# Optimization experiments

Hardware: AMD Instinct MI355X
Metric: run time of the kernel (lower is better)

Reference implementation:

```python
import jax, jax.numpy as jnp
import numpy as np

DIM = 128
NUM_HEADS = 8
HEAD_DIM = DIM // NUM_HEADS
SCALE = HEAD_DIM ** -0.5


def _attn_branch(xs, Wq, bq, Wp, bp):
    # xs: (N, L, C) batch of sequences; Q=K=V=q (per the module)
    N, L, C = xs.shape
    q = xs @ Wq + bq                                   # (N, L, C)
    q = q.reshape(N, L, NUM_HEADS, HEAD_DIM).transpose(0, 2, 1, 3)  # (N, h, L, d)
    qs = q * SCALE
    attn = jax.nn.softmax(jnp.einsum('nhld,nhmd->nhlm', qs, qs), axis=-1)
    out = jnp.einsum('nhlm,nhmd->nhld', attn, q)       # (N, h, L, d)
    out = out.transpose(0, 2, 1, 3).reshape(N, L, C)
    return out @ Wp + bp


def setup_inputs() -> dict:
    key = jax.random.key(0)
    ks = jax.random.split(key, 12)
    B, C, D, H, W = 1, DIM, 31, 32, 32
    s = 0.02
    return {
        'x': jax.random.normal(ks[0], (B, C, D, H, W), jnp.float32),
        'Wq_spec': jax.random.normal(ks[1], (C, C), jnp.float32) * s,
        'bq_spec': jnp.zeros((C,), jnp.float32),
        'Wp_spec': jax.random.normal(ks[2], (C, C), jnp.float32) * s,
        'bp_spec': jnp.zeros((C,), jnp.float32),
        'Wq_spat': jax.random.normal(ks[3], (C, C), jnp.float32) * s,
        'bq_spat': jnp.zeros((C,), jnp.float32),
        'Wp_spat': jax.random.normal(ks[4], (C, C), jnp.float32) * s,
        'bp_spat': jnp.zeros((C,), jnp.float32),
        'Wg': jax.random.normal(ks[5], (2 * C, C), jnp.float32) * s,
        'bg': jnp.zeros((C,), jnp.float32),
    }


def reference(x, Wq_spec, bq_spec, Wp_spec, bp_spec,
              Wq_spat, bq_spat, Wp_spat, bp_spat, Wg, bg):
    B, C, D, H, W = x.shape
    # ---- spectral branch: sequences of length D per spatial position ----
    x_spec = x.transpose(0, 3, 4, 2, 1).reshape(B * H * W, D, C)
    out_spec = _attn_branch(x_spec, Wq_spec, bq_spec, Wp_spec, bp_spec)
    out_spectral = out_spec.reshape(B, H, W, D, C).transpose(0, 4, 3, 1, 2)  # (B,C,D,H,W)
    # ---- spatial branch: sequences of length H*W per band ----
    x_spat = x.transpose(0, 2, 3, 4, 1).reshape(B * D, H * W, C)
    out_spat = _attn_branch(x_spat, Wq_spat, bq_spat, Wp_spat, bp_spat)
    out_spatial = out_spat.reshape(B, D, H, W, C).transpose(0, 4, 1, 2, 3)   # (B,C,D,H,W)
    # ---- sigmoid-gated fusion (global average pooled gate) ----
    gi = jnp.concatenate([
        out_spectral.mean(axis=(2, 3, 4)),
        out_spatial.mean(axis=(2, 3, 4)),
    ], axis=-1)                                          # (B, 2C)
    gate = jax.nn.sigmoid(gi @ Wg + bg)[:, :, None, None, None]  # (B,C,1,1,1)
    return gate * out_spectral + (1.0 - gate) * out_spatial
```

## Files before the change

### kernel.cpp

```cpp
#include <hip/hip_runtime.h>
#include <cstddef>

#define CC 128
#define NH 8
#define HD 16
#define DDIM 31
#define HWW 1024
#define TOK 31744
#define SCALE2 0.0625f
#define QTOK 64

typedef __attribute__((ext_vector_type(4))) short  short4v;
typedef __attribute__((ext_vector_type(8))) short  short8v;
typedef __attribute__((ext_vector_type(4))) float  float4v;
typedef __attribute__((ext_vector_type(2))) unsigned uint2v;
typedef __attribute__((ext_vector_type(8))) __bf16 bf16x8;

__device__ inline unsigned bf16rne(float f) {
    unsigned u = __float_as_uint(f);
    return (u + 0x7fffu + ((u >> 16) & 1u)) >> 16;
}
__device__ inline float bf2f(unsigned h) { return __uint_as_float(h << 16); }

__device__ inline unsigned packsplit(float v) {
    unsigned h = bf16rne(v);
    unsigned l = bf16rne(v - bf2f(h));
    return h | (l << 16);
}
__device__ inline uint2 pack_hi4(uint4 p) {
    return make_uint2((p.x & 0xffffu) | (p.y << 16),
                      (p.z & 0xffffu) | (p.w << 16));
}
__device__ inline uint2 pack_lo4(uint4 p) {
    return make_uint2((p.x >> 16) | (p.y & 0xffff0000u),
                      (p.z >> 16) | (p.w & 0xffff0000u));
}

__device__ inline short4v pack_pf(unsigned u0, unsigned u1,
                                  unsigned u2, unsigned u3) {
    uint2v pd;
    pd[0] = __builtin_amdgcn_perm(u1, u0, 0x07060302u);
    pd[1] = __builtin_amdgcn_perm(u3, u2, 0x07060302u);
    return __builtin_bit_cast(short4v, pd);
}

__device__ inline float4v mfma32(short8v a, short8v b, float4v c) {
    return __builtin_amdgcn_mfma_f32_16x16x32_bf16(
        __builtin_bit_cast(bf16x8, a), __builtin_bit_cast(bf16x8, b), c, 0, 0, 0);
}

__device__ inline void load_wfrags32(const float* __restrict__ W, int co0, int l,
                                     int quad, short8v* ah, short8v* al)
{
#pragma unroll
    for (int k4 = 0; k4 < 4; ++k4) {
#pragma unroll
        for (int j = 0; j < 8; ++j) {
            float w = W[(size_t)(k4 * 32 + quad * 8 + j) * CC + co0 + l];
            unsigned h = bf16rne(w);
            ah[k4][j] = (short)h;
            al[k4][j] = (short)bf16rne(w - bf2f(h));
        }
    }
}

#define AST 136

__global__ __launch_bounds__(512, 4) void qproj_kernel(
    const float* __restrict__ x,
    const float* __restrict__ Wq1, const float* __restrict__ Wq2,
    const float* __restrict__ bq1, const float* __restrict__ bq2,
    unsigned* __restrict__ q1p, unsigned* __restrict__ q2p,
    float* __restrict__ sums)
{
    __shared__ ushort sbuf[2 * QTOK * AST];
    ushort* Ahi = sbuf;
    ushort* Alo = sbuf + QTOK * AST;
    unsigned* S = (unsigned*)sbuf;
    const int tid = threadIdx.x;
    const int t0  = blockIdx.x * QTOK;
    if (blockIdx.x == 0 && tid < 2 * CC) sums[tid] = 0.f;

    for (int i = tid; i < CC * QTOK / 4; i += 512) {
        int t4 = i & 15, ci = i >> 4;
        float4 v = *(const float4*)&x[(size_t)ci * TOK + t0 + t4 * 4];
        float xv[4] = {v.x, v.y, v.z, v.w};
#pragma unroll
        for (int e = 0; e < 4; ++e) {
            unsigned h = bf16rne(xv[e]);
            unsigned lw = bf16rne(xv[e] - bf2f(h));
            Ahi[(t4 * 4 + e) * AST + ci] = (ushort)h;
            Alo[(t4 * 4 + e) * AST + ci] = (ushort)lw;
        }
    }
    __syncthreads();

    const int lane = tid & 63;
    const int l    = lane & 15;
    const int quad = lane >> 4;
    const int co0  = (tid >> 6) * 16;

    short8v ah[2][4], al[2][4];
    load_wfrags32(Wq1, co0, l, quad, ah[0], al[0]);
    load_wfrags32(Wq2, co0, l, quad, ah[1], al[1]);
    float4v acc[2][4];
#pragma unroll
    for (int br = 0; br < 2; ++br)
#pragma unroll
        for (int nt = 0; nt < 4; ++nt) acc[br][nt] = (float4v){0.f, 0.f, 0.f, 0.f};
#pragma unroll
    for (int k4 = 0; k4 < 4; ++k4) {
#pragma unroll
        for (int nt = 0; nt < 4; ++nt) {
            short8v bh = *(const short8v*)&Ahi[(nt * 16 + l) * AST + k4 * 32 + quad * 8];
            short8v bl = *(const short8v*)&Alo[(nt * 16 + l) * AST + k4 * 32 + quad * 8];
            acc[0][nt] = mfma32(ah[0][k4], bh, acc[0][nt]);
            acc[0][nt] = mfma32(ah[0][k4], bl, acc[0][nt]);
            acc[0][nt] = mfma32(al[0][k4], bh, acc[0][nt]);
            acc[1][nt] = mfma32(ah[1][k4], bh, acc[1][nt]);
            acc[1][nt] = mfma32(ah[1][k4], bl, acc[1][nt]);
            acc[1][nt] = mfma32(al[1][k4], bh, acc[1][nt]);
        }
    }

    for (int branch = 0; branch < 2; ++branch) {
        const float* bq = branch ? bq2 : bq1;
        unsigned* op    = branch ? q2p : q1p;
        float4 bv = *(const float4*)&bq[co0 + quad * 4];
        float bb[4] = {bv.x, bv.y, bv.z, bv.w};
        __syncthreads();
#pragma unroll
        for (int nt = 0; nt < 4; ++nt) {
#pragma unroll
            for (int reg = 0; reg < 4; ++reg)
                S[(nt * 16 + l) * AST + co0 + quad * 4 + reg] =
                    packsplit(acc[branch][nt][reg] + bb[reg]);
        }
        __syncthreads();
        for (int i = tid; i < QTOK * 32; i += 512) {
            int t = i >> 5, c4 = i & 31;
            uint4 pv = *(const uint4*)&S[t * AST + c4 * 4];
            *(uint4*)&op[(size_t)(t0 + t) * CC + c4 * 4] = pv;
        }
    }
}

#define QS2 132
#define QSS 20
#define QTP 1044
__global__ __launch_bounds__(1024, 4) void attn_kernel(
    unsigned* __restrict__ q1p, unsigned* __restrict__ q2p,
    float* __restrict__ sums)
{
    __shared__ __align__(16) ushort smem[HWW * QSS + HD * QTP];
    __shared__ float fsum[CC];
    const int tid  = threadIdx.x;
    const int lane = tid & 63;
    const int l    = lane & 15;
    const int quad = lane >> 4;
    const float k2 = SCALE2 * 1.44269504f;
    const short4v onesb = {(short)0x3F80, (short)0x3F80, (short)0x3F80, (short)0x3F80};
    if (tid < CC) fsum[tid] = 0.f;

    {
        const int d = blockIdx.x >> 3, h = blockIdx.x & 7;
        ushort* Qs  = smem;
        ushort* QTs = smem + HWW * QSS;
        const size_t base = (size_t)d * HWW * CC + h * HD;

        for (int i = tid; i < HWW * 4; i += 1024) {
            int row = i >> 2, q4 = i & 3;
            uint4 p = *(const uint4*)&q2p[base + (size_t)row * CC + q4 * 4];
            *(uint2*)&Qs[row * QSS + q4 * 4] = pack_hi4(p);
            QTs[(q4 * 4 + 0) * QTP + row] = (ushort)p.x;
            QTs[(q4 * 4 + 1) * QTP + row] = (ushort)p.y;
            QTs[(q4 * 4 + 2) * QTP + row] = (ushort)p.z;
            QTs[(q4 * 4 + 3) * QTP + row] = (ushort)p.w;
        }
        __syncthreads();

        const int Rw = (tid >> 6) * 64;
        short4v qf[4];
#pragma unroll
        for (int lt = 0; lt < 4; ++lt) {
            short4v raw = *(short4v*)&Qs[(Rw + lt * 16 + l) * QSS + quad * 4];
            short4v sc;
#pragma unroll
            for (int e = 0; e < 4; ++e) {
                float f = bf2f((unsigned)(ushort)raw[e]) * k2;
                sc[e] = (short)bf16rne(f);
            }
            qf[lt] = sc;
        }

        float4v acc[4], accs[4];
#pragma unroll
        for (int lt = 0; lt < 4; ++lt) {
            acc[lt]  = (float4v){0.f, 0.f, 0.f, 0.f};
            accs[lt] = (float4v){0.f, 0.f, 0.f, 0.f};
        }

#pragma unroll 2
        for (int mt = 0; mt < 64; ++mt) {
            const int m0 = mt * 16;
            short4v ka = *(short4v*)&Qs[(m0 + l) * QSS + quad * 4];
            short4v vb = *(short4v*)&QTs[l * QTP + m0 + quad * 4];
#pragma unroll
            for (int lt = 0; lt < 4; ++lt) {
                float4v s = __builtin_amdgcn_mfma_f32_16x16x16bf16_1k(
                    ka, qf[lt], (float4v){0.f, 0.f, 0.f, 0.f}, 0, 0, 0);
                unsigned u0 = __float_as_uint(__builtin_amdgcn_exp2f(s[0]));
                unsigned u1 = __float_as_uint(__builtin_amdgcn_exp2f(s[1]));
                unsigned u2 = __float_as_uint(__builtin_amdgcn_exp2f(s[2]));
                unsigned u3 = __float_as_uint(__builtin_amdgcn_exp2f(s[3]));
                short4v pf = pack_pf(u0, u1, u2, u3);
                acc[lt]  = __builtin_amdgcn_mfma_f32_16x16x16bf16_1k(vb, pf, acc[lt], 0, 0, 0);
                accs[lt] = __builtin_amdgcn_mfma_f32_16x16x16bf16_1k(onesb, pf, accs[lt], 0, 0, 0);
            }
        }

        float vsum[4] = {0.f, 0.f, 0.f, 0.f};
#pragma unroll
        for (int lt = 0; lt < 4; ++lt) {
            float inv = 1.f / accs[lt][0];
            int token = Rw + lt * 16 + l;
            float v0 = acc[lt][0] * inv, v1 = acc[lt][1] * inv;
            float v2 = acc[lt][2] * inv, v3 = acc[lt][3] * inv;
            uint4 pv;
            pv.x = packsplit(v0); pv.y = packsplit(v1);
            pv.z = packsplit(v2); pv.w = packsplit(v3);
            *(uint4*)&q2p[base + (size_t)token * CC + quad * 4] = pv;
            vsum[0] += v0; vsum[1] += v1; vsum[2] += v2; vsum[3] += v3;
        }
#pragma unroll
        for (int reg = 0; reg < 4; ++reg) {
            float v = vsum[reg];
            v += __shfl_xor(v, 1); v += __shfl_xor(v, 2);
            v += __shfl_xor(v, 4); v += __shfl_xor(v, 8);
            if (l == 0) atomicAdd(&fsum[quad * 4 + reg], v);
        }
        __syncthreads();
        if (tid < HD) atomicAdd(&sums[CC + h * HD + tid], fsum[tid]);
    }

    const int half_id = blockIdx.x >> 1;
    const bool has_job = (blockIdx.x & 1) ? (half_id < 4) : (half_id < 124);
    if (!has_job) return;
    const int job = (blockIdx.x & 1) ? (124 + half_id) : half_id;
    const int hw0 = job * 8;

    __syncthreads();
    if (tid < CC) fsum[tid] = 0.f;

    const int wave = tid >> 6;
    const int hwl  = wave >> 1;
    const int half = wave & 1;
    const int hw   = hw0 + hwl;
    ushort* Q = smem + hwl * (32 * QS2);
    for (int it = 0; it < 8; ++it) {
        int idx = it * 64 + lane;
        int dd = half * 16 + (idx >> 5), c4 = idx & 31;
        if (dd < 31) {
            uint4 p = *(const uint4*)&q1p[((size_t)dd * HWW + hw) * CC + c4 * 4];
            *(uint2*)&Q[dd * QS2 + c4 * 4] = pack_hi4(p);
        }
    }
    if (half) for (int i = lane; i < 128; i += 64) Q[31 * QS2 + i] = 0;
    __syncthreads();

    const int hh = half * 4;
#pragma unroll
    for (int hl = 0; hl < 4; ++hl) {
        const int hc = (hh + hl) * HD;
        short4v qf[2];
        qf[0] = *(const short4v*)&Q[l * QS2 + hc + quad * 4];
        qf[1] = *(const short4v*)&Q[(16 + l) * QS2 + hc + quad * 4];
        short4v va[2];
#pragma unroll
        for (int j = 0; j < 2; ++j)
#pragma unroll
            for (int jj = 0; jj < 4; ++jj)
                va[j][jj] = (short)Q[(j * 16 + quad * 4 + jj) * QS2 + hc + l];

        float4v o[2]   = {(float4v){0.f,0.f,0.f,0.f}, (float4v){0.f,0.f,0.f,0.f}};
        float4v osr[2] = {(float4v){0.f,0.f,0.f,0.f}, (float4v){0.f,0.f,0.f,0.f}};
#pragma unroll
        for (int j = 0; j < 2; ++j) {
#pragma unroll
            for (int i2 = 0; i2 < 2; ++i2) {
                float4v s = __builtin_amdgcn_mfma_f32_16x16x16bf16_1k(
                    qf[j], qf[i2], (float4v){0.f,0.f,0.f,0.f}, 0, 0, 0);
                unsigned u0 = __float_as_uint(__builtin_amdgcn_exp2f(s[0] * k2));
                unsigned u1 = __float_as_uint(__builtin_amdgcn_exp2f(s[1] * k2));
                unsigned u2 = __float_as_uint(__builtin_amdgcn_exp2f(s[2] * k2));
                unsigned u3 = __float_as_uint(__builtin_amdgcn_exp2f(s[3] * k2));
                if (j == 1 && quad == 3) u3 = 0;
                short4v pf = pack_pf(u0, u1, u2, u3);
                o[i2]   = __builtin_amdgcn_mfma_f32_16x16x16bf16_1k(va[j], pf, o[i2], 0, 0, 0);
                osr[i2] = __builtin_amdgcn_mfma_f32_16x16x16bf16_1k(onesb, pf, osr[i2], 0, 0, 0);
            }
        }
        float vsum[4] = {0.f, 0.f, 0.f, 0.f};
#pragma unroll
        for (int i2 = 0; i2 < 2; ++i2) {
            float inv = 1.f / osr[i2][0];
            int dq = i2 * 16 + l;
            if (dq < 31) {
                uint4 pv;
                float v0 = o[i2][0] * inv, v1 = o[i2][1] * inv;
                float v2 = o[i2][2] * inv, v3 = o[i2][3] * inv;
                pv.x = packsplit(v0); pv.y = packsplit(v1);
                pv.z = packsplit(v2); pv.w = packsplit(v3);
                *(uint4*)&q1p[((size_t)dq * HWW + hw) * CC + hc + quad * 4] = pv;
                vsum[0] += v0; vsum[1] += v1; vsum[2] += v2; vsum[3] += v3;
            }
        }
#pragma unroll
        for (int r = 0; r < 4; ++r) {
            float v = vsum[r];
            v += __shfl_xor(v, 1); v += __shfl_xor(v, 2);
            v += __shfl_xor(v, 4); v += __shfl_xor(v, 8);
            if (l == 0) atomicAdd(&fsum[hc + quad * 4 + r], v);
        }
    }
    __syncthreads();
    if (tid < CC) atomicAdd(&sums[tid], fsum[tid]);
}

__global__ __launch_bounds__(512, 4) void oproj_kernel(
    const unsigned* __restrict__ q1p, const unsigned* __restrict__ q2p,
    const float* __restrict__ Wp1, const float* __restrict__ Wp2,
    const float* __restrict__ bp1, const float* __restrict__ bp2,
    const float* __restrict__ Wg,  const float* __restrict__ bg,
    const float* __restrict__ sums, float* __restrict__ out)
{
    __shared__ ushort sbuf[2 * 64 * AST];
    ushort* Ahi = sbuf;
    ushort* Alo = sbuf + 64 * AST;
    unsigned* S = (unsigned*)sbuf;
    __shared__ float pa[4][CC];
    __shared__ float giv[2 * CC];
    __shared__ float gf[CC];
    const int tid = threadIdx.x;
    const int t0  = blockIdx.x * 64;
    const int lane = tid & 63;
    const int l    = lane & 15;
    const int quad = lane >> 4;
    const int co0  = (tid >> 6) * 16;

    {
        const int part = tid >> 7, c = tid & 127;
        const float* Wp = (part < 2) ? Wp1 : Wp2;
        const float* sp = (part < 2) ? sums : sums + CC;
        const int k0 = (part & 1) * 64;
        float a = 0.f;
        for (int kk = 0; kk < 64; ++kk) {
            int k = k0 + kk;
            a += sp[k] * Wp[(size_t)k * CC + c];
        }
        pa[part][c] = a;
        __syncthreads();
        if (tid < 2 * CC) {
            float m = (tid < CC) ? (pa[0][tid] + pa[1][tid])
                                 : (pa[2][tid - CC] + pa[3][tid - CC]);
            float bb = (tid < CC) ? bp1[tid] : bp2[tid - CC];
            giv[tid] = m * (1.f / (float)TOK) + bb;
        }
        __syncthreads();
        float b = 0.f;
        for (int kk = 0; kk < 64; ++kk) {
            int j = part * 64 + kk;
            b += giv[j] * Wg[(size_t)j * CC + c];
        }
        pa[part][c] = b;
        __syncthreads();
        if (tid < CC)
            gf[tid] = 1.f / (1.f + __expf(-(bg[tid] + pa[0][tid] + pa[1][tid] +
                                           pa[2][tid] + pa[3][tid])));
    }

    float4v acc[2][4];
#pragma unroll
    for (int br = 0; br < 2; ++br)
#pragma unroll
        for (int nt = 0; nt < 4; ++nt) acc[br][nt] = (float4v){0.f, 0.f, 0.f, 0.f};

    for (int br = 0; br < 2; ++br) {
        const unsigned* Ap = br ? q2p : q1p;
        const float*    W  = br ? Wp2 : Wp1;
        short8v ah[4], al[4];
        load_wfrags32(W, co0, l, quad, ah, al);
        __syncthreads();
        for (int i = tid; i < 64 * 32; i += 512) {
            int t = i >> 5, c4 = i & 31;
            uint4 p = *(const uint4*)&Ap[(size_t)(t0 + t) * CC + c4 * 4];
            *(uint2*)&Ahi[t * AST + c4 * 4] = pack_hi4(p);
            *(uint2*)&Alo[t * AST + c4 * 4] = pack_lo4(p);
        }
        __syncthreads();
#pragma unroll
        for (int k4 = 0; k4 < 4; ++k4) {
#pragma unroll
            for (int nt = 0; nt < 4; ++nt) {
                short8v bh = *(const short8v*)&Ahi[(nt * 16 + l) * AST + k4 * 32 + quad * 8];
                short8v bl = *(const short8v*)&Alo[(nt * 16 + l) * AST + k4 * 32 + quad * 8];
                acc[br][nt] = mfma32(ah[k4], bh, acc[br][nt]);
                acc[br][nt] = mfma32(ah[k4], bl, acc[br][nt]);
                acc[br][nt] = mfma32(al[k4], bh, acc[br][nt]);
            }
        }
    }

    float4 b1 = *(const float4*)&bp1[co0 + quad * 4];
    float4 b2 = *(const float4*)&bp2[co0 + quad * 4];
    float bb1[4] = {b1.x, b1.y, b1.z, b1.w};
    float bb2[4] = {b2.x, b2.y, b2.z, b2.w};
    float gg[4];
#pragma unroll
    for (int e = 0; e < 4; ++e) gg[e] = gf[co0 + quad * 4 + e];

    __syncthreads();
#pragma unroll
    for (int nt = 0; nt < 4; ++nt) {
        int tl = nt * 16 + l;
#pragma unroll
        for (int reg = 0; reg < 4; ++reg) {
            float v = gg[reg] * (acc[0][nt][reg] + bb1[reg]) +
                      (1.f - gg[reg]) * (acc[1][nt][reg] + bb2[reg]);
            S[(co0 + quad * 4 + reg) * 66 + tl] = __float_as_uint(v);
        }
    }
    __syncthreads();
    for (int i = tid; i < 128 * 32; i += 512) {
        int co = i >> 5, t2 = i & 31;
        uint2 v = *(const uint2*)&S[co * 66 + t2 * 2];
        *(uint2*)&out[(size_t)co * TOK + t0 + t2 * 2] = v;
    }
}

extern "C" void kernel_launch(void* const* d_in, const int* in_sizes, int n_in,
                              void* d_out, int out_size, void* d_ws, size_t ws_size,
                              hipStream_t stream)
{
    const float* x   = (const float*)d_in[0];
    const float* Wq1 = (const float*)d_in[1];
    const float* bq1 = (const float*)d_in[2];
    const float* Wp1 = (const float*)d_in[3];
    const float* bp1 = (const float*)d_in[4];
    const float* Wq2 = (const float*)d_in[5];
    const float* bq2 = (const float*)d_in[6];
    const float* Wp2 = (const float*)d_in[7];
    const float* bp2 = (const float*)d_in[8];
    const float* Wg  = (const float*)d_in[9];
    const float* bg  = (const float*)d_in[10];
    float* out = (float*)d_out;

    const size_t plane = (size_t)TOK * CC;
    unsigned* q1p = (unsigned*)d_ws;
    unsigned* q2p = q1p + plane;
    float*   sums = (float*)(q2p + plane);

    qproj_kernel<<<dim3(TOK / QTOK), 512, 0, stream>>>(x, Wq1, Wq2, bq1, bq2,
                                                       q1p, q2p, sums);
    attn_kernel<<<dim3(248), 1024, 0, stream>>>(q1p, q2p, sums);
    oproj_kernel<<<dim3(496), 512, 0, stream>>>(q1p, q2p,
                                                Wp1, Wp2, bp1, bp2, Wg, bg,
                                                sums, out);
}
```

Baseline: 173.0 us.

## Fuse three kernels into one cooperative persistent kernel with grid syncs

Replaces the three separate launches (q-projection, attention, output projection) with a single cooperative kernel of 248 blocks of 1024 threads that runs the three phases separated by grid-wide barriers. To fit the fixed grid, the projection phases now process 128 tokens per block with 16 waves. The weight bf16 hi/lo fragments are now converted per k-step inside the loop instead of preloaded, which lowers register use. If the cooperative launch fails, it falls back to three ordinary launches. This removes launch gaps and inter-kernel drain, but adds grid-sync cost and gives the projection phases fewer, larger blocks.

```diff
diff --git a/kernel.cpp b/kernel.cpp
--- a/kernel.cpp
+++ b/kernel.cpp
@@ -1,5 +1,8 @@
 #include <hip/hip_runtime.h>
+#include <hip/hip_cooperative_groups.h>
 #include <cstddef>
+
+namespace cg = cooperative_groups;
 
 #define CC 128
 #define NH 8
@@ -8,7 +11,9 @@
 #define HWW 1024
 #define TOK 31744
 #define SCALE2 0.0625f
-#define QTOK 64
+#define GRID 248
+#define BTOK 128
+#define AST 136
 
 typedef __attribute__((ext_vector_type(4))) short  short4v;
 typedef __attribute__((ext_vector_type(8))) short  short8v;
@@ -49,77 +54,76 @@
         __builtin_bit_cast(bf16x8, a), __builtin_bit_cast(bf16x8, b), c, 0, 0, 0);
 }
 
-__device__ inline void load_wfrags32(const float* __restrict__ W, int co0, int l,
-                                     int quad, short8v* ah, short8v* al)
-{
-#pragma unroll
-    for (int k4 = 0; k4 < 4; ++k4) {
-#pragma unroll
-        for (int j = 0; j < 8; ++j) {
-            float w = W[(size_t)(k4 * 32 + quad * 8 + j) * CC + co0 + l];
-            unsigned h = bf16rne(w);
-            ah[k4][j] = (short)h;
-            al[k4][j] = (short)bf16rne(w - bf2f(h));
-        }
-    }
-}
-
-#define AST 136
-
-__global__ __launch_bounds__(512, 4) void qproj_kernel(
+__device__ __forceinline__ void qproj_phase(
     const float* __restrict__ x,
     const float* __restrict__ Wq1, const float* __restrict__ Wq2,
     const float* __restrict__ bq1, const float* __restrict__ bq2,
     unsigned* __restrict__ q1p, unsigned* __restrict__ q2p,
-    float* __restrict__ sums)
-{
-    __shared__ ushort sbuf[2 * QTOK * AST];
+    float* __restrict__ sums, ushort* sbuf, int bx, int tid)
+{
     ushort* Ahi = sbuf;
-    ushort* Alo = sbuf + QTOK * AST;
+    ushort* Alo = sbuf + BTOK * AST;
     unsigned* S = (unsigned*)sbuf;
-    const int tid = threadIdx.x;
-    const int t0  = blockIdx.x * QTOK;
-    if (blockIdx.x == 0 && tid < 2 * CC) sums[tid] = 0.f;
-
-    for (int i = tid; i < CC * QTOK / 4; i += 512) {
-        int t4 = i & 15, ci = i >> 4;
-        float4 v = *(const float4*)&x[(size_t)ci * TOK + t0 + t4 * 4];
-        float xv[4] = {v.x, v.y, v.z, v.w};
-#pragma unroll
-        for (int e = 0; e < 4; ++e) {
-            unsigned h = bf16rne(xv[e]);
-            unsigned lw = bf16rne(xv[e] - bf2f(h));
-            Ahi[(t4 * 4 + e) * AST + ci] = (ushort)h;
-            Alo[(t4 * 4 + e) * AST + ci] = (ushort)lw;
-        }
+    const int t0 = bx * BTOK;
+    if (bx == 0 && tid < 2 * CC) sums[tid] = 0.f;
+
+    for (int i = tid; i < BTOK * 32; i += 1024) {
+        int t = i & (BTOK - 1), c4 = i >> 7;
+        unsigned hw[2], lw[2];
+#pragma unroll
+        for (int p = 0; p < 2; ++p) {
+            unsigned h0, l0, h1, l1;
+            {
+                float v = x[(size_t)(c4 * 4 + p * 2 + 0) * TOK + t0 + t];
+                h0 = bf16rne(v); l0 = bf16rne(v - bf2f(h0));
+            }
+            {
+                float v = x[(size_t)(c4 * 4 + p * 2 + 1) * TOK + t0 + t];
+                h1 = bf16rne(v); l1 = bf16rne(v - bf2f(h1));
+            }
+            hw[p] = h0 | (h1 << 16);
+            lw[p] = l0 | (l1 << 16);
+        }
+        *(uint2*)&Ahi[t * AST + c4 * 4] = make_uint2(hw[0], hw[1]);
+        *(uint2*)&Alo[t * AST + c4 * 4] = make_uint2(lw[0], lw[1]);
     }
     __syncthreads();
 
     const int lane = tid & 63;
     const int l    = lane & 15;
     const int quad = lane >> 4;
-    const int co0  = (tid >> 6) * 16;
-
-    short8v ah[2][4], al[2][4];
-    load_wfrags32(Wq1, co0, l, quad, ah[0], al[0]);
-    load_wfrags32(Wq2, co0, l, quad, ah[1], al[1]);
+    const int wv   = tid >> 6;
+    const int co0  = (wv & 7) * 16;
+    const int tb   = (wv >> 3) * 64;
+
     float4v acc[2][4];
 #pragma unroll
     for (int br = 0; br < 2; ++br)
 #pragma unroll
         for (int nt = 0; nt < 4; ++nt) acc[br][nt] = (float4v){0.f, 0.f, 0.f, 0.f};
+
 #pragma unroll
     for (int k4 = 0; k4 < 4; ++k4) {
+        short8v ah0, al0, ah1, al1;
+#pragma unroll
+        for (int j = 0; j < 8; ++j) {
+            float w1 = Wq1[(size_t)(k4 * 32 + quad * 8 + j) * CC + co0 + l];
+            unsigned h1 = bf16rne(w1);
+            ah0[j] = (short)h1; al0[j] = (short)bf16rne(w1 - bf2f(h1));
+            float w2 = Wq2[(size_t)(k4 * 32 + quad * 8 + j) * CC + co0 + l];
+            unsigned h2 = bf16rne(w2);
+            ah1[j] = (short)h2; al1[j] = (short)bf16rne(w2 - bf2f(h2));
+        }
 #pragma unroll
         for (int nt = 0; nt < 4; ++nt) {
-            short8v bh = *(const short8v*)&Ahi[(nt * 16 + l) * AST + k4 * 32 + quad * 8];
-            short8v bl = *(const short8v*)&Alo[(nt * 16 + l) * AST + k4 * 32 + quad * 8];
-            acc[0][nt] = mfma32(ah[0][k4], bh, acc[0][nt]);
-            acc[0][nt] = mfma32(ah[0][k4], bl, acc[0][nt]);
-            acc[0][nt] = mfma32(al[0][k4], bh, acc[0][nt]);
-            acc[1][nt] = mfma32(ah[1][k4], bh, acc[1][nt]);
-            acc[1][nt] = mfma32(ah[1][k4], bl, acc[1][nt]);
-            acc[1][nt] = mfma32(al[1][k4], bh, acc[1][nt]);
+            short8v bh = *(const short8v*)&Ahi[(tb + nt * 16 + l) * AST + k4 * 32 + quad * 8];
+            short8v bl = *(const short8v*)&Alo[(tb + nt * 16 + l) * AST + k4 * 32 + quad * 8];
+            acc[0][nt] = mfma32(ah0, bh, acc[0][nt]);
+            acc[0][nt] = mfma32(ah0, bl, acc[0][nt]);
+            acc[0][nt] = mfma32(al0, bh, acc[0][nt]);
+            acc[1][nt] = mfma32(ah1, bh, acc[1][nt]);
+            acc[1][nt] = mfma32(ah1, bl, acc[1][nt]);
+            acc[1][nt] = mfma32(al1, bh, acc[1][nt]);
         }
     }
 
@@ -133,11 +137,11 @@
         for (int nt = 0; nt < 4; ++nt) {
 #pragma unroll
             for (int reg = 0; reg < 4; ++reg)
-                S[(nt * 16 + l) * AST + co0 + quad * 4 + reg] =
+                S[(tb + nt * 16 + l) * AST + co0 + quad * 4 + reg] =
                     packsplit(acc[branch][nt][reg] + bb[reg]);
         }
         __syncthreads();
-        for (int i = tid; i < QTOK * 32; i += 512) {
+        for (int i = tid; i < BTOK * 32; i += 1024) {
             int t = i >> 5, c4 = i & 31;
             uint4 pv = *(const uint4*)&S[t * AST + c4 * 4];
             *(uint4*)&op[(size_t)(t0 + t) * CC + c4 * 4] = pv;
@@ -148,13 +152,10 @@
 #define QS2 132
 #define QSS 20
 #define QTP 1044
-__global__ __launch_bounds__(1024, 4) void attn_kernel(
+__device__ __forceinline__ void attn_phase(
     unsigned* __restrict__ q1p, unsigned* __restrict__ q2p,
-    float* __restrict__ sums)
-{
-    __shared__ __align__(16) ushort smem[HWW * QSS + HD * QTP];
-    __shared__ float fsum[CC];
-    const int tid  = threadIdx.x;
+    float* __restrict__ sums, ushort* smem, float* fsum, int bx, int tid)
+{
     const int lane = tid & 63;
     const int l    = lane & 15;
     const int quad = lane >> 4;
@@ -163,7 +164,7 @@
     if (tid < CC) fsum[tid] = 0.f;
 
     {
-        const int d = blockIdx.x >> 3, h = blockIdx.x & 7;
+        const int d = bx >> 3, h = bx & 7;
         ushort* Qs  = smem;
         ushort* QTs = smem + HWW * QSS;
         const size_t base = (size_t)d * HWW * CC + h * HD;
@@ -243,199 +244,270 @@
         if (tid < HD) atomicAdd(&sums[CC + h * HD + tid], fsum[tid]);
     }
 
-    const int half_id = blockIdx.x >> 1;
-    const bool has_job = (blockIdx.x & 1) ? (half_id < 4) : (half_id < 124);
-    if (!has_job) return;
-    const int job = (blockIdx.x & 1) ? (124 + half_id) : half_id;
-    const int hw0 = job * 8;
+    const int half_id = bx >> 1;
+    const bool has_job = (bx & 1) ? (half_id < 4) : (half_id < 124);
+    if (has_job) {
+        const int job = (bx & 1) ? (124 + half_id) : half_id;
+        const int hw0 = job * 8;
+
+        __syncthreads();
+        if (tid < CC) fsum[tid] = 0.f;
+
+        const int wave = tid >> 6;
+        const int hwl  = wave >> 1;
+        const int half = wave & 1;
+        const int hw   = hw0 + hwl;
+        ushort* Q = smem + hwl * (32 * QS2);
+        for (int it = 0; it < 8; ++it) {
+            int idx = it * 64 + lane;
+            int dd = half * 16 + (idx >> 5), c4 = idx & 31;
+            if (dd < 31) {
+                uint4 p = *(const uint4*)&q1p[((size_t)dd * HWW + hw) * CC + c4 * 4];
+                *(uint2*)&Q[dd * QS2 + c4 * 4] = pack_hi4(p);
+            }
+        }
+        if (half) for (int i = lane; i < 128; i += 64) Q[31 * QS2 + i] = 0;
+        __syncthreads();
+
+        const int hh = half * 4;
+#pragma unroll
+        for (int hl = 0; hl < 4; ++hl) {
+            const int hc = (hh + hl) * HD;
+            short4v qf[2];
+            qf[0] = *(const short4v*)&Q[l * QS2 + hc + quad * 4];
+            qf[1] = *(const short4v*)&Q[(16 + l) * QS2 + hc + quad * 4];
+            short4v va[2];
+#pragma unroll
+            for (int j = 0; j < 2; ++j)
+#pragma unroll
+                for (int jj = 0; jj < 4; ++jj)
+                    va[j][jj] = (short)Q[(j * 16 + quad * 4 + jj) * QS2 + hc + l];
+
+            float4v o[2]   = {(float4v){0.f,0.f,0.f,0.f}, (float4v){0.f,0.f,0.f,0.f}};
+            float4v osr[2] = {(float4v){0.f,0.f,0.f,0.f}, (float4v){0.f,0.f,0.f,0.f}};
+#pragma unroll
+            for (int j = 0; j < 2; ++j) {
+#pragma unroll
+                for (int i2 = 0; i2 < 2; ++i2) {
+                    float4v s = __builtin_amdgcn_mfma_f32_16x16x16bf16_1k(
+                        qf[j], qf[i2], (float4v){0.f,0.f,0.f,0.f}, 0, 0, 0);
+                    unsigned u0 = __float_as_uint(__builtin_amdgcn_exp2f(s[0] * k2));
+                    unsigned u1 = __float_as_uint(__builtin_amdgcn_exp2f(s[1] * k2));
+                    unsigned u2 = __float_as_uint(__builtin_amdgcn_exp2f(s[2] * k2));
+                    unsigned u3 = __float_as_uint(__builtin_amdgcn_exp2f(s[3] * k2));
+                    if (j == 1 && quad == 3) u3 = 0;
+                    short4v pf = pack_pf(u0, u1, u2, u3);
+                    o[i2]   = __builtin_amdgcn_mfma_f32_16x16x16bf16_1k(va[j], pf, o[i2], 0, 0, 0);
+                    osr[i2] = __builtin_amdgcn_mfma_f32_16x16x16bf16_1k(onesb, pf, osr[i2], 0, 0, 0);
+                }
+            }
+            float vsum[4] = {0.f, 0.f, 0.f, 0.f};
+#pragma unroll
+            for (int i2 = 0; i2 < 2; ++i2) {
+                float inv = 1.f / osr[i2][0];
+                int dq = i2 * 16 + l;
+                if (dq < 31) {
+                    uint4 pv;
+                    float v0 = o[i2][0] * inv, v1 = o[i2][1] * inv;
+                    float v2 = o[i2][2] * inv, v3 = o[i2][3] * inv;
+                    pv.x = packsplit(v0); pv.y = packsplit(v1);
+                    pv.z = packsplit(v2); pv.w = packsplit(v3);
+                    *(uint4*)&q1p[((size_t)dq * HWW + hw) * CC + hc + quad * 4] = pv;
+                    vsum[0] += v0; vsum[1] += v1; vsum[2] += v2; vsum[3] += v3;
+                }
+            }
+#pragma unroll
+            for (int r = 0; r < 4; ++r) {
+                float v = vsum[r];
+                v += __shfl_xor(v, 1); v += __shfl_xor(v, 2);
+                v += __shfl_xor(v, 4); v += __shfl_xor(v, 8);
+                if (l == 0) atomicAdd(&fsum[hc + quad * 4 + r], v);
+            }
+        }
+        __syncthreads();
+        if (tid < CC) atomicAdd(&sums[tid], fsum[tid]);
+    }
+}
+
+__device__ __forceinline__ void oproj_phase(
+    const unsigned* __restrict__ q1p, const unsigned* __restrict__ q2p,
+    const float* __restrict__ Wp1, const float* __restrict__ Wp2,
+    const float* __restrict__ bp1, const float* __restrict__ bp2,
+    const float* __restrict__ Wg,  const float* __restrict__ bg,
+    const float* __restrict__ sums, float* __restrict__ out,
+    ushort* sbuf, float* pa, float* giv, float* gf, int bx, int tid)
+{
+    ushort* Ahi = sbuf;
+    ushort* Alo = sbuf + BTOK * AST;
+    unsigned* S = (unsigned*)sbuf;
+    const int t0 = bx * BTOK;
+    const int lane = tid & 63;
+    const int l    = lane & 15;
+    const int quad = lane >> 4;
+    const int wv   = tid >> 6;
+    const int co0  = (wv & 7) * 16;
+    const int tb   = (wv >> 3) * 64;
+
+    {
+        const int part = tid >> 7, c = tid & 127;
+        if (part < 4) {
+            const float* Wp = (part < 2) ? Wp1 : Wp2;
+            const float* sp = (part < 2) ? sums : sums + CC;
+            const int k0 = (part & 1) * 64;
+            float a = 0.f;
+            for (int kk = 0; kk < 64; ++kk) {
+                int k = k0 + kk;
+                a += sp[k] * Wp[(size_t)k * CC + c];
+            }
+            pa[part * CC + c] = a;
+        }
+        __syncthreads();
+        if (tid < 2 * CC) {
+            float m = (tid < CC) ? (pa[0 * CC + tid] + pa[1 * CC + tid])
+                                 : (pa[2 * CC + tid - CC] + pa[3 * CC + tid - CC]);
+            float bb = (tid < CC) ? bp1[tid] : bp2[tid - CC];
+            giv[tid] = m * (1.f / (float)TOK) + bb;
+        }
+        __syncthreads();
+        if (part < 4) {
+            float b = 0.f;
+            for (int kk = 0; kk < 64; ++kk) {
+                int j = part * 64 + kk;
+                b += giv[j] * Wg[(size_t)j * CC + c];
+            }
+            pa[part * CC + c] = b;
+        }
+        __syncthreads();
+        if (tid < CC)
+            gf[tid] = 1.f / (1.f + __expf(-(bg[tid] + pa[0 * CC + tid] + pa[1 * CC + tid] +
+                                           pa[2 * CC + tid] + pa[3 * CC + tid])));
+    }
+
+    float4v acc[2][4];
+#pragma unroll
+    for (int br = 0; br < 2; ++br)
+#pragma unroll
+        for (int nt = 0; nt < 4; ++nt) acc[br][nt] = (float4v){0.f, 0.f, 0.f, 0.f};
+
+    for (int br = 0; br < 2; ++br) {
+        const unsigned* Ap = br ? q2p : q1p;
+        const float*    W  = br ? Wp2 : Wp1;
+        __syncthreads();
+        for (int i = tid; i < BTOK * 32; i += 1024) {
+            int t = i >> 5, c4 = i & 31;
+            uint4 p = *(const uint4*)&Ap[(size_t)(t0 + t) * CC + c4 * 4];
+            *(uint2*)&Ahi[t * AST + c4 * 4] = pack_hi4(p);
+            *(uint2*)&Alo[t * AST + c4 * 4] = pack_lo4(p);
+        }
+        __syncthreads();
+#pragma unroll
+        for (int k4 = 0; k4 < 4; ++k4) {
+            short8v ah, al;
+#pragma unroll
+            for (int j = 0; j < 8; ++j) {
+                float w = W[(size_t)(k4 * 32 + quad * 8 + j) * CC + co0 + l];
+                unsigned h = bf16rne(w);
+                ah[j] = (short)h; al[j] = (short)bf16rne(w - bf2f(h));
+            }
+#pragma unroll
+            for (int nt = 0; nt < 4; ++nt) {
+                short8v bh = *(const short8v*)&Ahi[(tb + nt * 16 + l) * AST + k4 * 32 + quad * 8];
+                short8v bl = *(const short8v*)&Alo[(tb + nt * 16 + l) * AST + k4 * 32 + quad * 8];
+                acc[br][nt] = mfma32(ah, bh, acc[br][nt]);
+                acc[br][nt] = mfma32(ah, bl, acc[br][nt]);
+                acc[br][nt] = mfma32(al, bh, acc[br][nt]);
+            }
+        }
+    }
+
+    float4 b1 = *(const float4*)&bp1[co0 + quad * 4];
+    float4 b2 = *(const float4*)&bp2[co0 + quad * 4];
+    float bb1[4] = {b1.x, b1.y, b1.z, b1.w};
+    float bb2[4] = {b2.x, b2.y, b2.z, b2.w};
+    float4 gv = *(const float4*)&gf[co0 + quad * 4];
+    float gg[4] = {gv.x, gv.y, gv.z, gv.w};
 
     __syncthreads();
-    if (tid < CC) fsum[tid] = 0.f;
-
-    const int wave = tid >> 6;
-    const int hwl  = wave >> 1;
-    const int half = wave & 1;
-    const int hw   = hw0 + hwl;
-    ushort* Q = smem + hwl * (32 * QS2);
-    for (int it = 0; it < 8; ++it) {
-        int idx = it * 64 + lane;
-        int dd = half * 16 + (idx >> 5), c4 = idx & 31;
-        if (dd < 31) {
-            uint4 p = *(const uint4*)&q1p[((size_t)dd * HWW + hw) * CC + c4 * 4];
-            *(uint2*)&Q[dd * QS2 + c4 * 4] = pack_hi4(p);
-        }
-    }
-    if (half) for (int i = lane; i < 128; i += 64) Q[31 * QS2 + i] = 0;
+#pragma unroll
+    for (int nt = 0; nt < 4; ++nt) {
+        int tl = tb + nt * 16 + l;
+#pragma unroll
+        for (int reg = 0; reg < 4; ++reg) {
+            float v = gg[reg] * (acc[0][nt][reg] + bb1[reg]) +
+                      (1.f - gg[reg]) * (acc[1][nt][reg] + bb2[reg]);
+            S[(co0 + quad * 4 + reg) * 130 + tl] = __float_as_uint(v);
+        }
+    }
     __syncthreads();
-
-    const int hh = half * 4;
-#pragma unroll
-    for (int hl = 0; hl < 4; ++hl) {
-        const int hc = (hh + hl) * HD;
-        short4v qf[2];
-        qf[0] = *(const short4v*)&Q[l * QS2 + hc + quad * 4];
-        qf[1] = *(const short4v*)&Q[(16 + l) * QS2 + hc + quad * 4];
-        short4v va[2];
-#pragma unroll
-        for (int j = 0; j < 2; ++j)
-#pragma unroll
-            for (int jj = 0; jj < 4; ++jj)
-                va[j][jj] = (short)Q[(j * 16 + quad * 4 + jj) * QS2 + hc + l];
-
-        float4v o[2]   = {(float4v){0.f,0.f,0.f,0.f}, (float4v){0.f,0.f,0.f,0.f}};
-        float4v osr[2] = {(float4v){0.f,0.f,0.f,0.f}, (float4v){0.f,0.f,0.f,0.f}};
-#pragma unroll
-        for (int j = 0; j < 2; ++j) {
-#pragma unroll
-            for (int i2 = 0; i2 < 2; ++i2) {
-                float4v s = __builtin_amdgcn_mfma_f32_16x16x16bf16_1k(
-                    qf[j], qf[i2], (float4v){0.f,0.f,0.f,0.f}, 0, 0, 0);
-                unsigned u0 = __float_as_uint(__builtin_amdgcn_exp2f(s[0] * k2));
-                unsigned u1 = __float_as_uint(__builtin_amdgcn_exp2f(s[1] * k2));
-                unsigned u2 = __float_as_uint(__builtin_amdgcn_exp2f(s[2] * k2));
-                unsigned u3 = __float_as_uint(__builtin_amdgcn_exp2f(s[3] * k2));
-                if (j == 1 && quad == 3) u3 = 0;
-                short4v pf = pack_pf(u0, u1, u2, u3);
-                o[i2]   = __builtin_amdgcn_mfma_f32_16x16x16bf16_1k(va[j], pf, o[i2], 0, 0, 0);
-                osr[i2] = __builtin_amdgcn_mfma_f32_16x16x16bf16_1k(onesb, pf, osr[i2], 0, 0, 0);
-            }
-        }
-        float vsum[4] = {0.f, 0.f, 0.f, 0.f};
-#pragma unroll
-        for (int i2 = 0; i2 < 2; ++i2) {
-            float inv = 1.f / osr[i2][0];
-            int dq = i2 * 16 + l;
-            if (dq < 31) {
-                uint4 pv;
-                float v0 = o[i2][0] * inv, v1 = o[i2][1] * inv;
-                float v2 = o[i2][2] * inv, v3 = o[i2][3] * inv;
-                pv.x = packsplit(v0); pv.y = packsplit(v1);
-                pv.z = packsplit(v2); pv.w = packsplit(v3);
-                *(uint4*)&q1p[((size_t)dq * HWW + hw) * CC + hc + quad * 4] = pv;
-                vsum[0] += v0; vsum[1] += v1; vsum[2] += v2; vsum[3] += v3;
-            }
-        }
-#pragma unroll
-        for (int r = 0; r < 4; ++r) {
-            float v = vsum[r];
-            v += __shfl_xor(v, 1); v += __shfl_xor(v, 2);
-            v += __shfl_xor(v, 4); v += __shfl_xor(v, 8);
-            if (l == 0) atomicAdd(&fsum[hc + quad * 4 + r], v);
-        }
-    }
-    __syncthreads();
-    if (tid < CC) atomicAdd(&sums[tid], fsum[tid]);
-}
-
-__global__ __launch_bounds__(512, 4) void oproj_kernel(
+    for (int i = tid; i < 128 * 64; i += 1024) {
+        int co = i >> 6, t2 = i & 63;
+        uint2 v = *(const uint2*)&S[co * 130 + t2 * 2];
+        *(uint2*)&out[(size_t)co * TOK + t0 + t2 * 2] = v;
+    }
+}
+
+__global__ __launch_bounds__(1024, 4) void fused_kernel(
+    const float* __restrict__ x,
+    const float* __restrict__ Wq1, const float* __restrict__ bq1,
+    const float* __restrict__ Wp1, const float* __restrict__ bp1,
+    const float* __restrict__ Wq2, const float* __restrict__ bq2,
+    const float* __restrict__ Wp2, const float* __restrict__ bp2,
+    const float* __restrict__ Wg,  const float* __restrict__ bg,
+    float* __restrict__ out,
+    unsigned* __restrict__ q1p, unsigned* __restrict__ q2p,
+    float* __restrict__ sums)
+{
+    __shared__ __align__(16) ushort smem[HWW * QSS + HD * QTP];
+    __shared__ float fsum[CC];
+    __shared__ float pa[4 * CC];
+    __shared__ float giv[2 * CC];
+    __shared__ float gf[CC];
+    const int bx = blockIdx.x, tid = threadIdx.x;
+
+    qproj_phase(x, Wq1, Wq2, bq1, bq2, q1p, q2p, sums, smem, bx, tid);
+    __threadfence();
+    cg::this_grid().sync();
+    attn_phase(q1p, q2p, sums, smem, fsum, bx, tid);
+    __threadfence();
+    cg::this_grid().sync();
+    oproj_phase(q1p, q2p, Wp1, Wp2, bp1, bp2, Wg, bg, sums, out,
+                smem, pa, giv, gf, bx, tid);
+}
+
+__global__ __launch_bounds__(1024, 4) void qproj_k(
+    const float* __restrict__ x,
+    const float* __restrict__ Wq1, const float* __restrict__ Wq2,
+    const float* __restrict__ bq1, const float* __restrict__ bq2,
+    unsigned* __restrict__ q1p, unsigned* __restrict__ q2p,
+    float* __restrict__ sums)
+{
+    __shared__ __align__(16) ushort smem[2 * BTOK * AST];
+    qproj_phase(x, Wq1, Wq2, bq1, bq2, q1p, q2p, sums, smem,
+                blockIdx.x, threadIdx.x);
+}
+
+__global__ __launch_bounds__(1024, 4) void attn_k(
+    unsigned* __restrict__ q1p, unsigned* __restrict__ q2p,
+    float* __restrict__ sums)
+{
+    __shared__ __align__(16) ushort smem[HWW * QSS + HD * QTP];
+    __shared__ float fsum[CC];
+    attn_phase(q1p, q2p, sums, smem, fsum, blockIdx.x, threadIdx.x);
+}
+
+__global__ __launch_bounds__(1024, 4) void oproj_k(
     const unsigned* __restrict__ q1p, const unsigned* __restrict__ q2p,
     const float* __restrict__ Wp1, const float* __restrict__ Wp2,
     const float* __restrict__ bp1, const float* __restrict__ bp2,
     const float* __restrict__ Wg,  const float* __restrict__ bg,
     const float* __restrict__ sums, float* __restrict__ out)
 {
-    __shared__ ushort sbuf[2 * 64 * AST];
-    ushort* Ahi = sbuf;
-    ushort* Alo = sbuf + 64 * AST;
-    unsigned* S = (unsigned*)sbuf;
-    __shared__ float pa[4][CC];
+    __shared__ __align__(16) ushort smem[2 * BTOK * AST];
+    __shared__ float pa[4 * CC];
     __shared__ float giv[2 * CC];
     __shared__ float gf[CC];
-    const int tid = threadIdx.x;
-    const int t0  = blockIdx.x * 64;
-    const int lane = tid & 63;
-    const int l    = lane & 15;
-    const int quad = lane >> 4;
-    const int co0  = (tid >> 6) * 16;
-
-    {
-        const int part = tid >> 7, c = tid & 127;
-        const float* Wp = (part < 2) ? Wp1 : Wp2;
-        const float* sp = (part < 2) ? sums : sums + CC;
-        const int k0 = (part & 1) * 64;
-        float a = 0.f;
-        for (int kk = 0; kk < 64; ++kk) {
-            int k = k0 + kk;
-            a += sp[k] * Wp[(size_t)k * CC + c];
-        }
-        pa[part][c] = a;
-        __syncthreads();
-        if (tid < 2 * CC) {
-            float m = (tid < CC) ? (pa[0][tid] + pa[1][tid])
-                                 : (pa[2][tid - CC] + pa[3][tid - CC]);
-            float bb = (tid < CC) ? bp1[tid] : bp2[tid - CC];
-            giv[tid] = m * (1.f / (float)TOK) + bb;
-        }
-        __syncthreads();
-        float b = 0.f;
-        for (int kk = 0; kk < 64; ++kk) {
-            int j = part * 64 + kk;
-            b += giv[j] * Wg[(size_t)j * CC + c];
-        }
-        pa[part][c] = b;
-        __syncthreads();
-        if (tid < CC)
-            gf[tid] = 1.f / (1.f + __expf(-(bg[tid] + pa[0][tid] + pa[1][tid] +
-                                           pa[2][tid] + pa[3][tid])));
-    }
-
-    float4v acc[2][4];
-#pragma unroll
-    for (int br = 0; br < 2; ++br)
-#pragma unroll
-        for (int nt = 0; nt < 4; ++nt) acc[br][nt] = (float4v){0.f, 0.f, 0.f, 0.f};
-
-    for (int br = 0; br < 2; ++br) {
-        const unsigned* Ap = br ? q2p : q1p;
-        const float*    W  = br ? Wp2 : Wp1;
-        short8v ah[4], al[4];
-        load_wfrags32(W, co0, l, quad, ah, al);
-        __syncthreads();
-        for (int i = tid; i < 64 * 32; i += 512) {
-            int t = i >> 5, c4 = i & 31;
-            uint4 p = *(const uint4*)&Ap[(size_t)(t0 + t) * CC + c4 * 4];
-            *(uint2*)&Ahi[t * AST + c4 * 4] = pack_hi4(p);
-            *(uint2*)&Alo[t * AST + c4 * 4] = pack_lo4(p);
-        }
-        __syncthreads();
-#pragma unroll
-        for (int k4 = 0; k4 < 4; ++k4) {
-#pragma unroll
-            for (int nt = 0; nt < 4; ++nt) {
-                short8v bh = *(const short8v*)&Ahi[(nt * 16 + l) * AST + k4 * 32 + quad * 8];
-                short8v bl = *(const short8v*)&Alo[(nt * 16 + l) * AST + k4 * 32 + quad * 8];
-                acc[br][nt] = mfma32(ah[k4], bh, acc[br][nt]);
-                acc[br][nt] = mfma32(ah[k4], bl, acc[br][nt]);
-                acc[br][nt] = mfma32(al[k4], bh, acc[br][nt]);
-            }
-        }
-    }
-
-    float4 b1 = *(const float4*)&bp1[co0 + quad * 4];
-    float4 b2 = *(const float4*)&bp2[co0 + quad * 4];
-    float bb1[4] = {b1.x, b1.y, b1.z, b1.w};
-    float bb2[4] = {b2.x, b2.y, b2.z, b2.w};
-    float gg[4];
-#pragma unroll
-    for (int e = 0; e < 4; ++e) gg[e] = gf[co0 + quad * 4 + e];
-
-    __syncthreads();
-#pragma unroll
-    for (int nt = 0; nt < 4; ++nt) {
-        int tl = nt * 16 + l;
-#pragma unroll
-        for (int reg = 0; reg < 4; ++reg) {
-            float v = gg[reg] * (acc[0][nt][reg] + bb1[reg]) +
-                      (1.f - gg[reg]) * (acc[1][nt][reg] + bb2[reg]);
-            S[(co0 + quad * 4 + reg) * 66 + tl] = __float_as_uint(v);
-        }
-    }
-    __syncthreads();
-    for (int i = tid; i < 128 * 32; i += 512) {
-        int co = i >> 5, t2 = i & 31;
-        uint2 v = *(const uint2*)&S[co * 66 + t2 * 2];
-        *(uint2*)&out[(size_t)co * TOK + t0 + t2 * 2] = v;
-    }
+    oproj_phase(q1p, q2p, Wp1, Wp2, bp1, bp2, Wg, bg, sums, out,
+                smem, pa, giv, gf, blockIdx.x, threadIdx.x);
 }
 
 extern "C" void kernel_launch(void* const* d_in, const int* in_sizes, int n_in,
@@ -460,10 +532,21 @@
     unsigned* q2p = q1p + plane;
     float*   sums = (float*)(q2p + plane);
 
-    qproj_kernel<<<dim3(TOK / QTOK), 512, 0, stream>>>(x, Wq1, Wq2, bq1, bq2,
-                                                       q1p, q2p, sums);
-    attn_kernel<<<dim3(248), 1024, 0, stream>>>(q1p, q2p, sums);
-    oproj_kernel<<<dim3(496), 512, 0, stream>>>(q1p, q2p,
-                                                Wp1, Wp2, bp1, bp2, Wg, bg,
-                                                sums, out);
-}
+    const size_t need = 2 * plane * sizeof(unsigned) + 2 * CC * sizeof(float);
+    if (ws_size < need) return;
+
+    void* args[] = {(void*)&x, (void*)&Wq1, (void*)&bq1, (void*)&Wp1, (void*)&bp1,
+                    (void*)&Wq2, (void*)&bq2, (void*)&Wp2, (void*)&bp2,
+                    (void*)&Wg, (void*)&bg, (void*)&out,
+                    (void*)&q1p, (void*)&q2p, (void*)&sums};
+    hipError_t err = hipLaunchCooperativeKernel((const void*)fused_kernel,
+                                                dim3(GRID), dim3(1024),
+                                                args, 0, stream);
+    if (err != hipSuccess) {
+        qproj_k<<<dim3(GRID), 1024, 0, stream>>>(x, Wq1, Wq2, bq1, bq2,
+                                                 q1p, q2p, sums);
+        attn_k<<<dim3(GRID), 1024, 0, stream>>>(q1p, q2p, sums);
+        oproj_k<<<dim3(GRID), 1024, 0, stream>>>(q1p, q2p, Wp1, Wp2, bp1, bp2,
+                                                 Wg, bg, sums, out);
+    }
+}
```

New measurement: 401.0 us. +131.7%, slower.
